# Optimization experiments

Measured on AMD Instinct MI355X. Metric: run time of the kernel, lower is better.

Reference implementation:

```python
import jax, jax.numpy as jnp
import numpy as np

N_NODES = 40000
N_EDGES = 640000
IN_CH = 64
HID = 128
N_LAYERS = 3


def _linear_params(key, shape_in, shape_out):
    kw, kb = jax.random.split(key)
    lim = 1.0 / np.sqrt(shape_in)
    W = jax.random.uniform(kw, (shape_in, shape_out), jnp.float32, -lim, lim)
    b = jax.random.uniform(kb, (shape_out,), jnp.float32, -lim, lim)
    return W, b


def setup_inputs() -> dict:
    key = jax.random.key(0)
    ks = jax.random.split(key, 32)
    edge_index = jax.random.randint(ks[0], (2, N_EDGES), 0, N_NODES, dtype=jnp.int64 if jax.config.jax_enable_x64 else jnp.int32)
    x = jax.random.normal(ks[1], (N_NODES, IN_CH), jnp.float32)
    pos = jax.random.normal(ks[2], (N_NODES, 3), jnp.float32)
    emb_W, emb_b = _linear_params(ks[3], IN_CH, HID)

    def stack(fn):
        outs = [fn(l) for l in range(N_LAYERS)]
        Ws = jnp.stack([o[0] for o in outs])
        bs = jnp.stack([o[1] for o in outs])
        return Ws, bs

    # edge MLP: Linear(2H+1, H), SiLU, Linear(H, H), SiLU
    edge_W1, edge_b1 = stack(lambda l: _linear_params(ks[4 + l], 2 * HID + 1, HID))
    edge_W2, edge_b2 = stack(lambda l: _linear_params(ks[8 + l], HID, HID))
    # node MLP: Linear(2H, H), SiLU, Linear(H, H)
    node_W1, node_b1 = stack(lambda l: _linear_params(ks[12 + l], 2 * HID, HID))
    node_W2, node_b2 = stack(lambda l: _linear_params(ks[16 + l], HID, HID))
    # pos MLP: Linear(H, H), SiLU, Linear(H, 1)
    pos_W1, pos_b1 = stack(lambda l: _linear_params(ks[20 + l], HID, HID))
    pos_W2, pos_b2 = stack(lambda l: _linear_params(ks[24 + l], HID, 1))
    return {
        "edge_index": edge_index, "x": x, "pos": pos,
        "emb_W": emb_W, "emb_b": emb_b,
        "edge_W1": edge_W1, "edge_b1": edge_b1, "edge_W2": edge_W2, "edge_b2": edge_b2,
        "node_W1": node_W1, "node_b1": node_b1, "node_W2": node_W2, "node_b2": node_b2,
        "pos_W1": pos_W1, "pos_b1": pos_b1, "pos_W2": pos_W2, "pos_b2": pos_b2,
    }


def reference(edge_index, x, pos, emb_W, emb_b,
              edge_W1, edge_b1, edge_W2, edge_b2,
              node_W1, node_b1, node_W2, node_b2,
              pos_W1, pos_b1, pos_W2, pos_b2):
    silu = jax.nn.silu
    N = x.shape[0]
    src, dst = edge_index[0], edge_index[1]  # messages flow src -> dst
    # node embedding
    h = x @ emb_W + emb_b  # [N, H]
    # in-degree for mean aggregation of position updates
    deg = jnp.clip(jax.ops.segment_sum(jnp.ones(src.shape[0], pos.dtype), dst, num_segments=N), 1.0)
    L = edge_W1.shape[0]
    for l in range(L):
        h_i = h[dst]            # [E, H] target features
        h_j = h[src]            # [E, H] source features
        rel = pos[dst] - pos[src]  # [E, 3]
        d2 = jnp.sum(rel * rel, axis=-1, keepdims=True)  # [E, 1] squared distance
        e_in = jnp.concatenate([h_i, h_j, d2], axis=-1)  # [E, 2H+1]
        m = silu(silu(e_in @ edge_W1[l] + edge_b1[l]) @ edge_W2[l] + edge_b2[l])  # [E, H]
        agg = jax.ops.segment_sum(m, dst, num_segments=N)  # [N, H]
        n_in = jnp.concatenate([h, agg], axis=-1)  # [N, 2H]
        h = silu(n_in @ node_W1[l] + node_b1[l]) @ node_W2[l] + node_b2[l]
        # equivariant position update: pos_i += mean_j (pos_i - pos_j) * phi_x(m_ij)
        w = silu(m @ pos_W1[l] + pos_b1[l]) @ pos_W2[l] + pos_b2[l]  # [E, 1]
        pos = pos + jax.ops.segment_sum(rel * w, dst, num_segments=N) / deg[:, None]
    return h, pos
```

## Files before the change

### kernel.cpp

```cpp
#include <hip/hip_runtime.h>
#include <hip/hip_bf16.h>

#define N_NODES 40000
#define N_EDGES 640000
#define IN_CH 64
#define HID 128
#define N_LAYERS 3

typedef unsigned short u16;
typedef unsigned int u32;

typedef __attribute__((ext_vector_type(8))) __bf16 bf16x8;
typedef __attribute__((ext_vector_type(4))) float float4v;

__device__ __forceinline__ float bf2f(u16 u) {
    union { u32 i; float f; } v; v.i = ((u32)u) << 16; return v.f;
}
__device__ __forceinline__ float bflo(u32 p) {
    union { u32 i; float f; } v; v.i = p << 16; return v.f;
}
__device__ __forceinline__ float bfhi(u32 p) {
    union { u32 i; float f; } v; v.i = p & 0xffff0000u; return v.f;
}
__device__ __forceinline__ u16 f2bf(float f) {
    union { float f; u32 i; } v; v.f = f;
    u32 i = v.i;
    u32 r = (i + 0x7fffu + ((i >> 16) & 1u)) >> 16;
    return (u16)r;
}
#if __has_builtin(__builtin_amdgcn_cvt_pk_bf16_f32)
typedef __attribute__((ext_vector_type(2))) __bf16 bf16x2_t;
__device__ __forceinline__ u32 pk2bf(float a, float b) {
    bf16x2_t p = __builtin_amdgcn_cvt_pk_bf16_f32(a, b);
    union { bf16x2_t v; u32 u; } c; c.v = p; return c.u;
}
#else
__device__ __forceinline__ u32 pk2bf(float a, float b) {
    return (u32)f2bf(a) | ((u32)f2bf(b) << 16);
}
#endif
__device__ __forceinline__ float silu_f(float x) {
    float d = 1.0f + __expf(-x);
#if __has_builtin(__builtin_amdgcn_rcpf)
    return x * __builtin_amdgcn_rcpf(d);
#else
    return __fdividef(x, d);
#endif
}

#define W_STRIDE 72
__device__ __forceinline__ void stage_w64(const u16* __restrict__ g, u16* s, int t,
                                          int chunk, int rowstride_u32) {
    const u32* gp = (const u32*)g;
    u32* sp = (u32*)s;
#pragma unroll
    for (int it = 0; it < 4; ++it) {
        int i4 = t + it * 256;
        int n = i4 >> 3, j = i4 & 7;
        *(uint4*)(sp + n * 36 + j * 4) = *(const uint4*)(gp + n * rowstride_u32 + chunk * 32 + j * 4);
    }
}

__device__ __forceinline__ int permch(int r) { return ((r & 15) << 3) | (r >> 4); }

__global__ void detect_kernel(const void* __restrict__ w_raw,
                              const void* __restrict__ eidx_raw,
                              int* __restrict__ flags) {
    __shared__ int s_big, s_hi;
    if (threadIdx.x == 0) { s_big = 0; s_hi = 0; }
    __syncthreads();
    const u16* w16 = (const u16*)w_raw;
    for (int i = threadIdx.x; i < 8192; i += blockDim.x) {
        float v = bf2f(w16[i]);
        if (!(fabsf(v) <= 1.0f)) s_big = 1;
    }
    const u32* e32 = (const u32*)eidx_raw;
    for (int i = threadIdx.x; i < 256; i += blockDim.x) {
        if (e32[2 * i + 1] != 0u) s_hi = 1;
    }
    __syncthreads();
    if (threadIdx.x == 0) {
        flags[0] = s_big ? 0 : 1;
        flags[1] = s_hi ? 0 : 1;
    }
}

__global__ void small_cvt_kernel(
    const void* __restrict__ embB_raw, const void* __restrict__ eB1_raw,
    const void* __restrict__ eB2_raw, const void* __restrict__ pB1_raw,
    const void* __restrict__ pB2_raw, const void* __restrict__ pW2_raw,
    const void* __restrict__ eW1_raw, const void* __restrict__ nB1_raw,
    const void* __restrict__ nB2_raw,
    float* __restrict__ dstf, const int* __restrict__ flags)
{
    int i = blockIdx.x * blockDim.x + threadIdx.x;
    if (i >= 2820) return;
    const void* src; int si;
    if (i < 128)       { src = embB_raw; si = i; }
    else if (i < 512)  { src = eB1_raw;  si = i - 128; }
    else if (i < 896)  { src = eB2_raw;  si = i - 512; }
    else if (i < 1280) { src = pB1_raw;  si = i - 896; }
    else if (i < 1284) { src = pB2_raw;  si = i - 1280; if (si >= 3) { dstf[i] = 0.f; return; } }
    else if (i < 1668) { src = pW2_raw;  si = i - 1284; }
    else if (i < 2052) { int j = i - 1668; src = eW1_raw; si = (j >> 7) * 32896 + 32768 + (j & 127); }
    else if (i < 2436) { src = nB1_raw;  si = i - 2052; }
    else               { src = nB2_raw;  si = i - 2436; }
    dstf[i] = flags[0] ? bf2f(((const u16*)src)[si]) : ((const float*)src)[si];
}

__global__ void wcvt_kernel(
    const void* __restrict__ eW1_raw, const void* __restrict__ eW2_raw,
    const void* __restrict__ pW1_raw, const void* __restrict__ nW1_raw,
    const void* __restrict__ nW2_raw, const void* __restrict__ embW_raw,
    u16* __restrict__ W1abt, u16* __restrict__ W2t, u16* __restrict__ pW1t,
    u16* __restrict__ nW1t, u16* __restrict__ nW2t, u16* __restrict__ embWt,
    const int* __restrict__ flags)
{
    int z = blockIdx.z, l = blockIdx.y;
    int i = blockIdx.x * blockDim.x + threadIdx.x;
    const void* src; u16* dst; int si, di;
    if (z == 0) {
        if (i >= 32768) return;
        int o = i >> 7, k = i & 127;
        int ch = permch(o & 127);
        si = l * 32896 + ((o < 128) ? (k * 128 + ch) : ((128 + k) * 128 + ch));
        src = eW1_raw; dst = W1abt; di = l * 32768 + i;
    } else if (z == 1) {
        if (i >= 16384) return;
        int n = i >> 7, k = i & 127;
        si = l * 16384 + k * 128 + permch(n); src = eW2_raw; dst = W2t; di = l * 16384 + i;
    } else if (z == 2) {
        if (i >= 16384) return;
        int n = i >> 7, k = i & 127;
        si = l * 16384 + k * 128 + n; src = pW1_raw; dst = pW1t; di = l * 16384 + i;
    } else if (z == 3) {
        if (i >= 32768) return;
        int n = i >> 8, k = i & 255;
        si = l * 32768 + k * 128 + permch(n); src = nW1_raw; dst = nW1t; di = l * 32768 + i;
    } else if (z == 4) {
        if (i >= 16384) return;
        int n = i >> 7, k = i & 127;
        si = l * 16384 + k * 128 + permch(n); src = nW2_raw; dst = nW2t; di = l * 16384 + i;
    } else {
        if (l != 0 || i >= 8192) return;
        int n = i >> 6, k = i & 63;
        si = k * 128 + permch(n); src = embW_raw; dst = embWt; di = i;
    }
    float v = flags[0] ? bf2f(((const u16*)src)[si]) : ((const float*)src)[si];
    dst[di] = f2bf(v);
}

__global__ void cnt_kernel(const void* __restrict__ eidx, int* __restrict__ cnt,
                           const int* __restrict__ flags) {
    int e = blockIdx.x * blockDim.x + threadIdx.x;
    if (e >= N_EDGES) return;
    int dn = flags[1] ? (int)((const long long*)eidx)[N_EDGES + e]
                      : ((const int*)eidx)[N_EDGES + e];
    atomicAdd(&cnt[dn], 1);
}

__global__ __launch_bounds__(1024) void scan_kernel(const int* __restrict__ cnt,
                                                    int* __restrict__ offs) {
    __shared__ int s_part[1024];
    const int t = threadIdx.x;
    const int base = t * 40;
    int sum = 0;
    for (int j = 0; j < 40; ++j) {
        int idx = base + j;
        sum += (idx < N_NODES) ? cnt[idx] : 0;
    }
    s_part[t] = sum;
    __syncthreads();
    for (int d = 1; d < 1024; d <<= 1) {
        int v = (t >= d) ? s_part[t - d] : 0;
        __syncthreads();
        s_part[t] += v;
        __syncthreads();
    }
    int run = (t == 0) ? 0 : s_part[t - 1];
    for (int j = 0; j < 40; ++j) {
        int idx = base + j;
        if (idx < N_NODES) { offs[idx] = run; run += cnt[idx]; }
    }
    if (t == 1023) offs[N_NODES] = run;
}

__global__ void scatter_kernel(const void* __restrict__ eidx,
                               const int* __restrict__ offs, int* __restrict__ cur,
                               int* __restrict__ ssrc, int* __restrict__ sdst,
                               const int* __restrict__ flags) {
    int e = blockIdx.x * blockDim.x + threadIdx.x;
    if (e >= N_EDGES) return;
    int sn, dn;
    if (flags[1]) {
        sn = (int)((const long long*)eidx)[e];
        dn = (int)((const long long*)eidx)[N_EDGES + e];
    } else {
        sn = ((const int*)eidx)[e];
        dn = ((const int*)eidx)[N_EDGES + e];
    }
    int p = offs[dn] + atomicAdd(&cur[dn], 1);
    ssrc[p] = sn;
    sdst[p] = dn;
}

__global__ void posinit_kernel(const void* __restrict__ pos_raw, float* __restrict__ posf,
                               const int* __restrict__ flags) {
    int i = blockIdx.x * blockDim.x + threadIdx.x;
    if (i < N_NODES * 3)
        posf[i] = flags[0] ? bf2f(((const u16*)pos_raw)[i]) : ((const float*)pos_raw)[i];
}

#define ACT_STRIDE 136

__global__ __launch_bounds__(256, 3) void embed_uv_kernel(
    const void* __restrict__ x_raw, const u16* __restrict__ embWt, const float* __restrict__ embB,
    const u16* __restrict__ W1abt, const float* __restrict__ b1,
    u16* __restrict__ h, u16* __restrict__ uv, const int* __restrict__ flags)
{
    __shared__ __align__(16) u16 s_x[64 * 72];
    __shared__ __align__(16) u16 s_h[64 * ACT_STRIDE];
    __shared__ __align__(16) u16 s_w[128 * W_STRIDE];

    const int t = threadIdx.x;
    const int n0 = blockIdx.x * 64;
    const int wv = t >> 6, lane = t & 63, quad = lane >> 4, li = lane & 15;
    const int rowA = wv * 16 + li;
    const int rowC = wv * 16 + quad * 4;

    {
        int el = t >> 2, pt4 = t & 3;
        u32* op = (u32*)s_x + el * 36 + pt4 * 8;
        if (flags[0]) {
            const u32* xp = (const u32*)x_raw + (size_t)(n0 + el) * 32 + pt4 * 8;
            *(uint4*)(op)     = *(const uint4*)(xp);
            *(uint4*)(op + 4) = *(const uint4*)(xp + 4);
        } else {
            const float* xp = (const float*)x_raw + (size_t)(n0 + el) * 64 + pt4 * 16;
#pragma unroll
            for (int j = 0; j < 8; ++j) op[j] = pk2bf(xp[2 * j], xp[2 * j + 1]);
        }
    }
    stage_w64(embWt, s_w, t, 0, 32);
    __syncthreads();

    float4v acc[8];
#pragma unroll
    for (int c = 0; c < 8; ++c) {
        float bias = embB[li * 8 + c];
#pragma unroll
        for (int r = 0; r < 4; ++r) acc[c][r] = bias;
    }
#pragma unroll
    for (int kk2 = 0; kk2 < 2; ++kk2) {
        const bf16x8 av = *(const bf16x8*)(s_x + rowA * 72 + kk2 * 32 + quad * 8);
#pragma unroll
        for (int c = 0; c < 8; ++c) {
            const bf16x8 bv = *(const bf16x8*)(s_w + (c * 16 + li) * W_STRIDE + kk2 * 32 + quad * 8);
            acc[c] = __builtin_amdgcn_mfma_f32_16x16x32_bf16(av, bv, acc[c], 0, 0, 0);
        }
    }
#pragma unroll
    for (int r = 0; r < 4; ++r) {
        u32 res[4];
#pragma unroll
        for (int c2 = 0; c2 < 4; ++c2)
            res[c2] = pk2bf(acc[2 * c2][r], acc[2 * c2 + 1][r]);
        *(uint4*)((u32*)s_h + (rowC + r) * (ACT_STRIDE / 2) + li * 4) = *(uint4*)res;
        *(uint4*)((u32*)h + (size_t)(n0 + rowC + r) * 64 + li * 4) = *(uint4*)res;
    }

    float4v a2[16];
#pragma unroll
    for (int ct = 0; ct < 16; ++ct) {
        float bias = (ct < 8) ? b1[li * 8 + ct] : 0.0f;
#pragma unroll
        for (int r = 0; r < 4; ++r) a2[ct][r] = bias;
    }
#pragma unroll
    for (int half = 0; half < 2; ++half) {
#pragma unroll
        for (int chunk = 0; chunk < 2; ++chunk) {
            __syncthreads();
            stage_w64(W1abt + half * 16384, s_w, t, chunk, 64);
            __syncthreads();
#pragma unroll
            for (int kk2 = 0; kk2 < 2; ++kk2) {
                const bf16x8 av = *(const bf16x8*)(s_h + rowA * ACT_STRIDE + chunk * 64 + kk2 * 32 + quad * 8);
#pragma unroll
                for (int c = 0; c < 8; ++c) {
                    const bf16x8 bv = *(const bf16x8*)(s_w + (c * 16 + li) * W_STRIDE + kk2 * 32 + quad * 8);
                    a2[half * 8 + c] = __builtin_amdgcn_mfma_f32_16x16x32_bf16(av, bv, a2[half * 8 + c], 0, 0, 0);
                }
            }
        }
    }
#pragma unroll
    for (int half = 0; half < 2; ++half) {
#pragma unroll
        for (int r = 0; r < 4; ++r) {
            u32 res[4];
#pragma unroll
            for (int c2 = 0; c2 < 4; ++c2)
                res[c2] = pk2bf(a2[half * 8 + 2 * c2][r], a2[half * 8 + 2 * c2 + 1][r]);
            *(uint4*)((u32*)uv + (size_t)(n0 + rowC + r) * 128 + half * 64 + li * 4) = *(uint4*)res;
        }
    }
}

#define TILE_E 64

__global__ __launch_bounds__(256, 4) void edge_mfma_kernel(
    const int* __restrict__ ssrc, const int* __restrict__ sdst,
    const u16* __restrict__ uv, const float* __restrict__ posf,
    const float* __restrict__ w1c_g,
    const u16* __restrict__ W2t, const float* __restrict__ b2,
    const u16* __restrict__ pW1t, const float* __restrict__ pb1,
    const float* __restrict__ pW2, const float* __restrict__ pb2,
    float* __restrict__ agg, float* __restrict__ pd)
{
    __shared__ __align__(16) u16 s_act[TILE_E * ACT_STRIDE];
    __shared__ __align__(16) u16 s_w[128 * W_STRIDE];
    __shared__ float s_w1c[128];
    __shared__ float s_d2[TILE_E];
    __shared__ float s_rel[TILE_E * 3];
    __shared__ int s_dstn[TILE_E];

    const int t = threadIdx.x;
    const int e0 = blockIdx.x * TILE_E;
    const int wv = t >> 6, lane = t & 63, quad = lane >> 4, li = lane & 15;
    const int rowA = wv * 16 + li;
    const int rowC = wv * 16 + quad * 4;

    {
        const int el = t >> 2, pt4 = t & 3;
        int eg = e0 + el;
        int dNg = sdst[eg], sNg = ssrc[eg];
        const uint4* up = (const uint4*)((const u32*)uv + (size_t)dNg * 128 + pt4 * 16);
        const uint4* vp = (const uint4*)((const u32*)uv + (size_t)sNg * 128 + 64 + pt4 * 16);
        uint4 uu[4], vv[4];
#pragma unroll
        for (int q4 = 0; q4 < 4; ++q4) { uu[q4] = up[q4]; vv[q4] = vp[q4]; }

        if (t < TILE_E) {
            int e = e0 + t;
            int sN = ssrc[e], dN = sdst[e];
            s_dstn[t] = dN;
            float r0 = posf[dN * 3 + 0] - posf[sN * 3 + 0];
            float r1 = posf[dN * 3 + 1] - posf[sN * 3 + 1];
            float r2 = posf[dN * 3 + 2] - posf[sN * 3 + 2];
            s_rel[t * 3 + 0] = r0; s_rel[t * 3 + 1] = r1; s_rel[t * 3 + 2] = r2;
            s_d2[t] = r0 * r0 + r1 * r1 + r2 * r2;
        }
        if (t < 128) s_w1c[t] = w1c_g[t];
        stage_w64(W2t, s_w, t, 0, 64);
        __syncthreads();

        float d2 = s_d2[el];
        u32* outp = (u32*)s_act + el * (ACT_STRIDE / 2) + pt4 * 16;
        const float* wc = s_w1c + pt4 * 32;
#pragma unroll
        for (int q4 = 0; q4 < 4; ++q4) {
            u32 res[4];
#pragma unroll
            for (int j = 0; j < 4; ++j) {
                u32 ua = ((const u32*)&uu[q4])[j], va = ((const u32*)&vv[q4])[j];
                int col = q4 * 8 + j * 2;
                float x0 = fmaf(d2, wc[col],     bflo(ua) + bflo(va));
                float x1 = fmaf(d2, wc[col + 1], bfhi(ua) + bfhi(va));
                res[j] = pk2bf(silu_f(x0), silu_f(x1));
            }
            *(uint4*)(outp + q4 * 4) = *(uint4*)res;
        }
    }
    __syncthreads();

    float4v acc[8];
#pragma unroll
    for (int c = 0; c < 8; ++c) {
        float bias = b2[li * 8 + c];
#pragma unroll
        for (int r = 0; r < 4; ++r) acc[c][r] = bias;
    }
#pragma unroll
    for (int p = 0; p < 2; ++p) {
        if (p) {
            __syncthreads();
            stage_w64(W2t, s_w, t, 1, 64);
            __syncthreads();
        }
#pragma unroll
        for (int kk2 = 0; kk2 < 2; ++kk2) {
            const bf16x8 av = *(const bf16x8*)(s_act + rowA * ACT_STRIDE + p * 64 + kk2 * 32 + quad * 8);
#pragma unroll
            for (int c = 0; c < 8; ++c) {
                const bf16x8 bv = *(const bf16x8*)(s_w + (c * 16 + li) * W_STRIDE + kk2 * 32 + quad * 8);
                acc[c] = __builtin_amdgcn_mfma_f32_16x16x32_bf16(av, bv, acc[c], 0, 0, 0);
            }
        }
    }
    __syncthreads();

#pragma unroll
    for (int r = 0; r < 4; ++r) {
        u32 res[4];
#pragma unroll
        for (int c2 = 0; c2 < 4; ++c2)
            res[c2] = pk2bf(silu_f(acc[2 * c2][r]), silu_f(acc[2 * c2 + 1][r]));
        *(uint4*)((u32*)s_act + (rowC + r) * (ACT_STRIDE / 2) + li * 4) = *(uint4*)res;
    }
    stage_w64(pW1t, s_w, t, 0, 64);
    __syncthreads();

    {
        int c32 = t & 63, grp = t >> 6;
        int r0 = grp * 16;
        float run0 = 0.f, run1 = 0.f;
        int cur = s_dstn[r0];
        for (int r = r0; r < r0 + 16; ++r) {
            int dn = s_dstn[r];
            if (dn != cur) {
                atomicAdd(&agg[(size_t)cur * HID + 2 * c32], run0);
                atomicAdd(&agg[(size_t)cur * HID + 2 * c32 + 1], run1);
                run0 = run1 = 0.f; cur = dn;
            }
            u32 mm = *((const u32*)s_act + r * (ACT_STRIDE / 2) + c32);
            run0 += bflo(mm);
            run1 += bfhi(mm);
        }
        atomicAdd(&agg[(size_t)cur * HID + 2 * c32], run0);
        atomicAdd(&agg[(size_t)cur * HID + 2 * c32 + 1], run1);
    }

#pragma unroll
    for (int c = 0; c < 8; ++c) {
        float bias = pb1[c * 16 + li];
#pragma unroll
        for (int r = 0; r < 4; ++r) acc[c][r] = bias;
    }
#pragma unroll
    for (int p = 0; p < 2; ++p) {
        if (p) {
            __syncthreads();
            stage_w64(pW1t, s_w, t, 1, 64);
            __syncthreads();
        }
#pragma unroll
        for (int kk2 = 0; kk2 < 2; ++kk2) {
            const bf16x8 av = *(const bf16x8*)(s_act + rowA * ACT_STRIDE + p * 64 + kk2 * 32 + quad * 8);
#pragma unroll
            for (int c = 0; c < 8; ++c) {
                const bf16x8 bv = *(const bf16x8*)(s_w + (c * 16 + li) * W_STRIDE + kk2 * 32 + quad * 8);
                acc[c] = __builtin_amdgcn_mfma_f32_16x16x32_bf16(av, bv, acc[c], 0, 0, 0);
            }
        }
    }
    float part[4] = {0.f, 0.f, 0.f, 0.f};
#pragma unroll
    for (int c = 0; c < 8; ++c) {
        float pw = pW2[c * 16 + li];
#pragma unroll
        for (int r = 0; r < 4; ++r) part[r] += silu_f(acc[c][r]) * pw;
    }
#pragma unroll
    for (int r = 0; r < 4; ++r) {
        part[r] += __shfl_xor(part[r], 1, 64);
        part[r] += __shfl_xor(part[r], 2, 64);
        part[r] += __shfl_xor(part[r], 4, 64);
        part[r] += __shfl_xor(part[r], 8, 64);
    }
    __syncthreads();
    if (li == 0) {
        float pb2v = pb2[0];
#pragma unroll
        for (int r = 0; r < 4; ++r) s_d2[rowC + r] = part[r] + pb2v;
    }
    __syncthreads();
    if (t < 12) {
        int a = t % 3, grp = t / 3;
        int r0 = grp * 16;
        float run = 0.f;
        int cur = s_dstn[r0];
        for (int r = r0; r < r0 + 16; ++r) {
            int dn = s_dstn[r];
            if (dn != cur) {
                atomicAdd(&pd[(size_t)cur * 3 + a], run);
                run = 0.f; cur = dn;
            }
            run += s_rel[r * 3 + a] * s_d2[r];
        }
        atomicAdd(&pd[(size_t)cur * 3 + a], run);
    }
}

#define A_STRIDE 264

__global__ __launch_bounds__(256, 3) void node_uv_kernel(
    const u16* __restrict__ h_in, float* __restrict__ agg,
    const u16* __restrict__ W1t, const float* __restrict__ b1,
    const u16* __restrict__ W2t, const float* __restrict__ b2,
    const u16* __restrict__ W1abt_nx, const float* __restrict__ b1_nx,
    u16* __restrict__ h_out, u16* __restrict__ uv,
    float* __restrict__ posf, float* __restrict__ pd, const int* __restrict__ cnt,
    void* __restrict__ outp, const int* __restrict__ flags, int do_out)
{
    __shared__ __align__(16) u16 s_a[64 * A_STRIDE];
    __shared__ __align__(16) u16 s_w[128 * W_STRIDE];

    const int t = threadIdx.x;
    const int n0 = blockIdx.x * 64;
    const int wv = t >> 6, lane = t & 63, quad = lane >> 4, li = lane & 15;
    const int rowA = wv * 16 + li;
    const int rowC = wv * 16 + quad * 4;

    {
        int nl = t >> 2, pt4 = t & 3;
        const uint4* hp = (const uint4*)((const u32*)h_in + (size_t)(n0 + nl) * 64 + pt4 * 16);
        u32* rowp = (u32*)s_a + nl * (A_STRIDE / 2) + pt4 * 16;
#pragma unroll
        for (int j = 0; j < 4; ++j) *(uint4*)(rowp + j * 4) = hp[j];
        float* ap = agg + (size_t)(n0 + nl) * HID + pt4 * 32;
        rowp += 64;
#pragma unroll
        for (int j = 0; j < 16; ++j) {
            float2 v = *(const float2*)(ap + j * 2);
            rowp[j] = pk2bf(v.x, v.y);
        }
        float4 z = {0.f, 0.f, 0.f, 0.f};
#pragma unroll
        for (int j = 0; j < 8; ++j) *(float4*)(ap + j * 4) = z;
    }
    stage_w64(W1t, s_w, t, 0, 128);
    __syncthreads();

    float4v acc[8];
#pragma unroll
    for (int c = 0; c < 8; ++c) {
        float bias = b1[li * 8 + c];
#pragma unroll
        for (int r = 0; r < 4; ++r) acc[c][r] = bias;
    }
#pragma unroll
    for (int p = 0; p < 4; ++p) {
        if (p) {
            __syncthreads();
            stage_w64(W1t, s_w, t, p, 128);
            __syncthreads();
        }
#pragma unroll
        for (int kk2 = 0; kk2 < 2; ++kk2) {
            const bf16x8 av = *(const bf16x8*)(s_a + rowA * A_STRIDE + p * 64 + kk2 * 32 + quad * 8);
#pragma unroll
            for (int c = 0; c < 8; ++c) {
                const bf16x8 bv = *(const bf16x8*)(s_w + (c * 16 + li) * W_STRIDE + kk2 * 32 + quad * 8);
                acc[c] = __builtin_amdgcn_mfma_f32_16x16x32_bf16(av, bv, acc[c], 0, 0, 0);
            }
        }
    }

    __syncthreads();
    u16* s_t1 = s_a;
#pragma unroll
    for (int r = 0; r < 4; ++r) {
        u32 res[4];
#pragma unroll
        for (int c2 = 0; c2 < 4; ++c2)
            res[c2] = pk2bf(silu_f(acc[2 * c2][r]), silu_f(acc[2 * c2 + 1][r]));
        *(uint4*)((u32*)s_t1 + (rowC + r) * (ACT_STRIDE / 2) + li * 4) = *(uint4*)res;
    }
    stage_w64(W2t, s_w, t, 0, 64);
    __syncthreads();

#pragma unroll
    for (int c = 0; c < 8; ++c) {
        float bias = b2[li * 8 + c];
#pragma unroll
        for (int r = 0; r < 4; ++r) acc[c][r] = bias;
    }
#pragma unroll
    for (int p = 0; p < 2; ++p) {
        if (p) {
            __syncthreads();
            stage_w64(W2t, s_w, t, 1, 64);
            __syncthreads();
        }
#pragma unroll
        for (int kk2 = 0; kk2 < 2; ++kk2) {
            const bf16x8 av = *(const bf16x8*)(s_t1 + rowA * ACT_STRIDE + p * 64 + kk2 * 32 + quad * 8);
#pragma unroll
            for (int c = 0; c < 8; ++c) {
                const bf16x8 bv = *(const bf16x8*)(s_w + (c * 16 + li) * W_STRIDE + kk2 * 32 + quad * 8);
                acc[c] = __builtin_amdgcn_mfma_f32_16x16x32_bf16(av, bv, acc[c], 0, 0, 0);
            }
        }
    }

    if (do_out) {
        if (flags[0]) {
#pragma unroll
            for (int r = 0; r < 4; ++r) {
                u32 res[4];
#pragma unroll
                for (int c2 = 0; c2 < 4; ++c2)
                    res[c2] = pk2bf(acc[2 * c2][r], acc[2 * c2 + 1][r]);
                *(uint4*)((u32*)outp + (size_t)(n0 + rowC + r) * 64 + li * 4) = *(uint4*)res;
            }
        } else {
#pragma unroll
            for (int r = 0; r < 4; ++r) {
                float* op = (float*)outp + (size_t)(n0 + rowC + r) * HID + li * 8;
                float4 lo = {acc[0][r], acc[1][r], acc[2][r], acc[3][r]};
                float4 hi = {acc[4][r], acc[5][r], acc[6][r], acc[7][r]};
                *(float4*)op = lo;
                *(float4*)(op + 4) = hi;
            }
        }
    } else {
#pragma unroll
        for (int r = 0; r < 4; ++r) {
            u32 res[4];
#pragma unroll
            for (int c2 = 0; c2 < 4; ++c2)
                res[c2] = pk2bf(acc[2 * c2][r], acc[2 * c2 + 1][r]);
            *(uint4*)((u32*)s_t1 + (rowC + r) * (ACT_STRIDE / 2) + li * 4) = *(uint4*)res;
            *(uint4*)((u32*)h_out + (size_t)(n0 + rowC + r) * 64 + li * 4) = *(uint4*)res;
        }
    }

    if (t < 192) {
        int nl = t / 3, a = t % 3;
        int n = n0 + nl;
        float dg = (float)cnt[n];
        dg = dg < 1.0f ? 1.0f : dg;
        float np = posf[n * 3 + a] + pd[n * 3 + a] / dg;
        posf[n * 3 + a] = np;
        pd[n * 3 + a] = 0.f;
        if (do_out) {
            if (flags[0]) ((u16*)outp)[(size_t)N_NODES * HID + n * 3 + a] = f2bf(np);
            else          ((float*)outp)[(size_t)N_NODES * HID + n * 3 + a] = np;
        }
    }

    if (do_out) return;

    float4v a2[16];
#pragma unroll
    for (int ct = 0; ct < 16; ++ct) {
        float bias = (ct < 8) ? b1_nx[li * 8 + ct] : 0.0f;
#pragma unroll
        for (int r = 0; r < 4; ++r) a2[ct][r] = bias;
    }
#pragma unroll
    for (int half = 0; half < 2; ++half) {
#pragma unroll
        for (int chunk = 0; chunk < 2; ++chunk) {
            __syncthreads();
            stage_w64(W1abt_nx + half * 16384, s_w, t, chunk, 64);
            __syncthreads();
#pragma unroll
            for (int kk2 = 0; kk2 < 2; ++kk2) {
                const bf16x8 av = *(const bf16x8*)(s_t1 + rowA * ACT_STRIDE + chunk * 64 + kk2 * 32 + quad * 8);
#pragma unroll
                for (int c = 0; c < 8; ++c) {
                    const bf16x8 bv = *(const bf16x8*)(s_w + (c * 16 + li) * W_STRIDE + kk2 * 32 + quad * 8);
                    a2[half * 8 + c] = __builtin_amdgcn_mfma_f32_16x16x32_bf16(av, bv, a2[half * 8 + c], 0, 0, 0);
                }
            }
        }
    }
#pragma unroll
    for (int half = 0; half < 2; ++half) {
#pragma unroll
        for (int r = 0; r < 4; ++r) {
            u32 res[4];
#pragma unroll
            for (int c2 = 0; c2 < 4; ++c2)
                res[c2] = pk2bf(a2[half * 8 + 2 * c2][r], a2[half * 8 + 2 * c2 + 1][r]);
            *(uint4*)((u32*)uv + (size_t)(n0 + rowC + r) * 128 + half * 64 + li * 4) = *(uint4*)res;
        }
    }
}

extern "C" void kernel_launch(void* const* d_in, const int* in_sizes, int n_in,
                              void* d_out, int out_size, void* d_ws, size_t ws_size,
                              hipStream_t stream) {
    (void)in_sizes; (void)n_in; (void)out_size; (void)ws_size;

    const void* eidx_raw = d_in[0];
    const void* x_raw    = d_in[1];
    const void* pos_raw  = d_in[2];
    const void* embW_raw = d_in[3];
    const void* embB_raw = d_in[4];
    const void* eW1_raw  = d_in[5];
    const void* eB1_raw  = d_in[6];
    const void* eW2_raw  = d_in[7];
    const void* eB2_raw  = d_in[8];
    const void* nW1_raw  = d_in[9];
    const void* nB1_raw  = d_in[10];
    const void* nW2_raw  = d_in[11];
    const void* nB2_raw  = d_in[12];
    const void* pW1_raw  = d_in[13];
    const void* pB1_raw  = d_in[14];
    const void* pW2_raw  = d_in[15];
    const void* pB2_raw  = d_in[16];

    float* ws   = (float*)d_ws;
    float* posf = ws;
    float* agg  = posf + (size_t)N_NODES * 3;
    float* pd   = agg + (size_t)N_NODES * HID;
    float* smallf = pd + (size_t)N_NODES * 3;
    float* embB = smallf;
    float* eB1f = smallf + 128;
    float* eB2f = smallf + 512;
    float* pB1f = smallf + 896;
    float* pB2f = smallf + 1280;
    float* pW2f = smallf + 1284;
    float* W1r  = smallf + 1668;
    float* nB1f = smallf + 2052;
    float* nB2f = smallf + 2436;

    u16* W1abt = (u16*)(smallf + 2820);
    u16* W2t   = W1abt + 3 * 256 * 128;
    u16* pW1t  = W2t + 3 * 128 * 128;
    u16* nW1t  = pW1t + 3 * 128 * 128;
    u16* nW2t  = nW1t + 3 * 128 * 256;
    u16* embWt = nW2t + 3 * 128 * 128;
    u16* h0    = embWt + 8192;
    u16* h1    = h0 + (size_t)N_NODES * HID;
    u16* uvb   = h1 + (size_t)N_NODES * HID;
    int* ssrc  = (int*)(uvb + (size_t)N_NODES * 256);
    int* sdst  = ssrc + N_EDGES;
    int* cnt   = sdst + N_EDGES;
    int* cur   = cnt + N_NODES;
    int* offs  = cur + N_NODES;
    int* flags = offs + N_NODES + 3;

    detect_kernel<<<1, 256, 0, stream>>>(embW_raw, eidx_raw, flags);
    small_cvt_kernel<<<12, 256, 0, stream>>>(embB_raw, eB1_raw, eB2_raw, pB1_raw, pB2_raw,
                                             pW2_raw, eW1_raw, nB1_raw, nB2_raw, smallf, flags);
    wcvt_kernel<<<dim3(128, 3, 6), 256, 0, stream>>>(
        eW1_raw, eW2_raw, pW1_raw, nW1_raw, nW2_raw, embW_raw,
        W1abt, W2t, pW1t, nW1t, nW2t, embWt, flags);

    hipMemsetAsync(cnt, 0, 2 * (size_t)N_NODES * sizeof(int), stream);
    cnt_kernel<<<(N_EDGES + 255) / 256, 256, 0, stream>>>(eidx_raw, cnt, flags);
    scan_kernel<<<1, 1024, 0, stream>>>(cnt, offs);
    scatter_kernel<<<(N_EDGES + 255) / 256, 256, 0, stream>>>(eidx_raw, offs, cur, ssrc, sdst, flags);

    posinit_kernel<<<(N_NODES * 3 + 255) / 256, 256, 0, stream>>>(pos_raw, posf, flags);
    hipMemsetAsync(agg, 0, ((size_t)N_NODES * HID + (size_t)N_NODES * 3) * sizeof(float), stream);

    embed_uv_kernel<<<N_NODES / 64, 256, 0, stream>>>(x_raw, embWt, embB, W1abt, eB1f, h0, uvb, flags);

    u16* hin = h0;
    u16* hout = h1;
    for (int l = 0; l < N_LAYERS; ++l) {
        int last = (l == N_LAYERS - 1);
        edge_mfma_kernel<<<N_EDGES / TILE_E, 256, 0, stream>>>(
            ssrc, sdst, uvb, posf,
            W1r + l * HID,
            W2t + (size_t)l * 128 * 128, eB2f + l * HID,
            pW1t + (size_t)l * 128 * 128, pB1f + l * HID,
            pW2f + l * HID, pB2f + l,
            agg, pd);
        node_uv_kernel<<<N_NODES / 64, 256, 0, stream>>>(
            hin, agg,
            nW1t + (size_t)l * 128 * 256, nB1f + l * HID,
            nW2t + (size_t)l * 128 * 128, nB2f + l * HID,
            W1abt + (size_t)(last ? 0 : (l + 1)) * 32768, eB1f + (last ? 0 : (l + 1)) * HID,
            hout, uvb,
            posf, pd, cnt,
            d_out, flags, last ? 1 : 0);
        u16* tmp = hin; hin = hout; hout = tmp;
    }
}
```

Before: 768.7 us.

## Make edge kernel wave-local and read MFMA weights directly from global memory

The shared-memory staging of the W2 and pos-MLP weight matrices and of the w1c vector is removed. MFMA B operands and w1c are now loaded straight from global memory, relying on L1/L2 caching. Each wave computes position/d2 data for its own 16 edges, so every block-wide __syncthreads becomes a compiler-only memory barrier and the aggregation loops are indexed per wave. This removes barrier stalls and LDS footprint, which may raise occupancy. The cost is higher-latency global loads inside the MFMA inner loops and repeated weight traffic per wave.

```diff
diff --git a/kernel.cpp b/kernel.cpp
--- a/kernel.cpp
+++ b/kernel.cpp
@@ -320,8 +320,6 @@
     float* __restrict__ agg, float* __restrict__ pd)
 {
     __shared__ __align__(16) u16 s_act[TILE_E * ACT_STRIDE];
-    __shared__ __align__(16) u16 s_w[128 * W_STRIDE];
-    __shared__ float s_w1c[128];
     __shared__ float s_d2[TILE_E];
     __shared__ float s_rel[TILE_E * 3];
     __shared__ int s_dstn[TILE_E];
@@ -332,48 +330,48 @@
     const int rowA = wv * 16 + li;
     const int rowC = wv * 16 + quad * 4;
 
+    if (lane < 16) {
+        int row = wv * 16 + lane;
+        int e = e0 + row;
+        int sN = ssrc[e], dN = sdst[e];
+        s_dstn[row] = dN;
+        float r0 = posf[dN * 3 + 0] - posf[sN * 3 + 0];
+        float r1 = posf[dN * 3 + 1] - posf[sN * 3 + 1];
+        float r2 = posf[dN * 3 + 2] - posf[sN * 3 + 2];
+        s_rel[row * 3 + 0] = r0; s_rel[row * 3 + 1] = r1; s_rel[row * 3 + 2] = r2;
+        s_d2[row] = r0 * r0 + r1 * r1 + r2 * r2;
+    }
+    asm volatile("" ::: "memory");
+
     {
         const int el = t >> 2, pt4 = t & 3;
-        int eg = e0 + el;
-        int dNg = sdst[eg], sNg = ssrc[eg];
-        const uint4* up = (const uint4*)((const u32*)uv + (size_t)dNg * 128 + pt4 * 16);
-        const uint4* vp = (const uint4*)((const u32*)uv + (size_t)sNg * 128 + 64 + pt4 * 16);
+        int e = e0 + el;
+        int dN = sdst[e], sN = ssrc[e];
+        const uint4* up = (const uint4*)((const u32*)uv + (size_t)dN * 128 + pt4 * 16);
+        const uint4* vp = (const uint4*)((const u32*)uv + (size_t)sN * 128 + 64 + pt4 * 16);
         uint4 uu[4], vv[4];
 #pragma unroll
         for (int q4 = 0; q4 < 4; ++q4) { uu[q4] = up[q4]; vv[q4] = vp[q4]; }
-
-        if (t < TILE_E) {
-            int e = e0 + t;
-            int sN = ssrc[e], dN = sdst[e];
-            s_dstn[t] = dN;
-            float r0 = posf[dN * 3 + 0] - posf[sN * 3 + 0];
-            float r1 = posf[dN * 3 + 1] - posf[sN * 3 + 1];
-            float r2 = posf[dN * 3 + 2] - posf[sN * 3 + 2];
-            s_rel[t * 3 + 0] = r0; s_rel[t * 3 + 1] = r1; s_rel[t * 3 + 2] = r2;
-            s_d2[t] = r0 * r0 + r1 * r1 + r2 * r2;
-        }
-        if (t < 128) s_w1c[t] = w1c_g[t];
-        stage_w64(W2t, s_w, t, 0, 64);
-        __syncthreads();
-
         float d2 = s_d2[el];
+        const float* wc = w1c_g + pt4 * 32;
         u32* outp = (u32*)s_act + el * (ACT_STRIDE / 2) + pt4 * 16;
-        const float* wc = s_w1c + pt4 * 32;
 #pragma unroll
         for (int q4 = 0; q4 < 4; ++q4) {
+            float wcv[8];
+            *(float4*)(wcv)     = *(const float4*)(wc + q4 * 8);
+            *(float4*)(wcv + 4) = *(const float4*)(wc + q4 * 8 + 4);
             u32 res[4];
 #pragma unroll
             for (int j = 0; j < 4; ++j) {
                 u32 ua = ((const u32*)&uu[q4])[j], va = ((const u32*)&vv[q4])[j];
-                int col = q4 * 8 + j * 2;
-                float x0 = fmaf(d2, wc[col],     bflo(ua) + bflo(va));
-                float x1 = fmaf(d2, wc[col + 1], bfhi(ua) + bfhi(va));
+                float x0 = fmaf(d2, wcv[2 * j],     bflo(ua) + bflo(va));
+                float x1 = fmaf(d2, wcv[2 * j + 1], bfhi(ua) + bfhi(va));
                 res[j] = pk2bf(silu_f(x0), silu_f(x1));
             }
             *(uint4*)(outp + q4 * 4) = *(uint4*)res;
         }
     }
-    __syncthreads();
+    asm volatile("" ::: "memory");
 
     float4v acc[8];
 #pragma unroll
@@ -384,22 +382,18 @@
     }
 #pragma unroll
     for (int p = 0; p < 2; ++p) {
-        if (p) {
-            __syncthreads();
-            stage_w64(W2t, s_w, t, 1, 64);
-            __syncthreads();
-        }
 #pragma unroll
         for (int kk2 = 0; kk2 < 2; ++kk2) {
             const bf16x8 av = *(const bf16x8*)(s_act + rowA * ACT_STRIDE + p * 64 + kk2 * 32 + quad * 8);
+            const u16* wb = W2t + (size_t)li * 128 + p * 64 + kk2 * 32 + quad * 8;
 #pragma unroll
             for (int c = 0; c < 8; ++c) {
-                const bf16x8 bv = *(const bf16x8*)(s_w + (c * 16 + li) * W_STRIDE + kk2 * 32 + quad * 8);
+                const bf16x8 bv = *(const bf16x8*)(wb + c * 2048);
                 acc[c] = __builtin_amdgcn_mfma_f32_16x16x32_bf16(av, bv, acc[c], 0, 0, 0);
             }
         }
     }
-    __syncthreads();
+    asm volatile("" ::: "memory");
 
 #pragma unroll
     for (int r = 0; r < 4; ++r) {
@@ -409,12 +403,11 @@
             res[c2] = pk2bf(silu_f(acc[2 * c2][r]), silu_f(acc[2 * c2 + 1][r]));
         *(uint4*)((u32*)s_act + (rowC + r) * (ACT_STRIDE / 2) + li * 4) = *(uint4*)res;
     }
-    stage_w64(pW1t, s_w, t, 0, 64);
-    __syncthreads();
+    asm volatile("" ::: "memory");
 
     {
-        int c32 = t & 63, grp = t >> 6;
-        int r0 = grp * 16;
+        int c32 = lane;
+        int r0 = wv * 16;
         float run0 = 0.f, run1 = 0.f;
         int cur = s_dstn[r0];
         for (int r = r0; r < r0 + 16; ++r) {
@@ -440,17 +433,13 @@
     }
 #pragma unroll
     for (int p = 0; p < 2; ++p) {
-        if (p) {
-            __syncthreads();
-            stage_w64(pW1t, s_w, t, 1, 64);
-            __syncthreads();
-        }
 #pragma unroll
         for (int kk2 = 0; kk2 < 2; ++kk2) {
             const bf16x8 av = *(const bf16x8*)(s_act + rowA * ACT_STRIDE + p * 64 + kk2 * 32 + quad * 8);
+            const u16* wb = pW1t + (size_t)li * 128 + p * 64 + kk2 * 32 + quad * 8;
 #pragma unroll
             for (int c = 0; c < 8; ++c) {
-                const bf16x8 bv = *(const bf16x8*)(s_w + (c * 16 + li) * W_STRIDE + kk2 * 32 + quad * 8);
+                const bf16x8 bv = *(const bf16x8*)(wb + c * 2048);
                 acc[c] = __builtin_amdgcn_mfma_f32_16x16x32_bf16(av, bv, acc[c], 0, 0, 0);
             }
         }
@@ -469,16 +458,16 @@
         part[r] += __shfl_xor(part[r], 4, 64);
         part[r] += __shfl_xor(part[r], 8, 64);
     }
-    __syncthreads();
+    asm volatile("" ::: "memory");
     if (li == 0) {
         float pb2v = pb2[0];
 #pragma unroll
         for (int r = 0; r < 4; ++r) s_d2[rowC + r] = part[r] + pb2v;
     }
-    __syncthreads();
-    if (t < 12) {
-        int a = t % 3, grp = t / 3;
-        int r0 = grp * 16;
+    asm volatile("" ::: "memory");
+    if (lane < 3) {
+        int a = lane;
+        int r0 = wv * 16;
         float run = 0.f;
         int cur = s_dstn[r0];
         for (int r = r0; r < r0 + 16; ++r) {
```

Result: slower. 1.397 ms (+81.8%).
